# Optimization experiments

Measured on AMD Instinct MI355X. Metric: run time of the kernel, lower is better.

Reference implementation:

```python
import jax, jax.numpy as jnp
import numpy as np

B, CH1, CH2, HID, T, E = 64, 3, 4, 16, 16384, 512

def setup_inputs() -> dict:
    key = jax.random.key(0)
    ks = jax.random.split(key, 12)
    s_t = 1.0 / np.sqrt(T)   # fan_in = input_dim for q/k/v projections
    s_e = 1.0 / np.sqrt(E)   # fan_in = embed_dim for out_proj
    return {
        "x":  jax.random.normal(ks[0], (B, 7, T), jnp.float32),
        "W1": jax.random.normal(ks[1], (HID, CH1), jnp.float32) / np.sqrt(CH1),
        "W2": jax.random.normal(ks[2], (HID, CH2), jnp.float32) / np.sqrt(CH2),
        "Wq": jax.random.normal(ks[3], (E, T), jnp.float32) * s_t,
        "bq": jnp.zeros((E,), jnp.float32),
        "Wk": jax.random.normal(ks[4], (E, T), jnp.float32) * s_t,
        "bk": jnp.zeros((E,), jnp.float32),
        "Wv": jax.random.normal(ks[5], (E, T), jnp.float32) * s_t,
        "bv": jnp.zeros((E,), jnp.float32),
        "Wo": jax.random.normal(ks[6], (T, E), jnp.float32) * s_e,
        "bo": jnp.zeros((T,), jnp.float32),
        "W3": jax.random.normal(ks[7], (CH1, HID), jnp.float32) / np.sqrt(HID),
    }

def reference(x, W1, W2, Wq, bq, Wk, bk, Wv, bv, Wo, bo, W3):
    p = x[:, :CH1]            # [B,3,T]  narrow(1,0,ch_1)
    c = x[:, 3:3 + CH2]       # [B,4,T]  narrow(1,3,ch_2)
    q = jnp.einsum('oc,bct->bot', W1, p)   # fc_1: [B,16,T]
    cc = jnp.einsum('oc,bct->bot', W2, c)  # fc_2: [B,16,T]
    # CrossAttention: Linears act on last dim (T -> E)
    Q = jnp.einsum('bct,et->bce', q, Wq) + bq    # [B,16,E]
    K = jnp.einsum('bct,et->bce', cc, Wk) + bk   # [B,16,E]
    V = jnp.einsum('bct,et->bce', cc, Wv) + bv   # [B,16,E]
    scale = 1.0 / np.sqrt(HID)                   # nch = 16 query channels
    attn_w = jax.nn.softmax(jnp.einsum('bce,bcf->bef', Q, K) * scale, axis=-1)  # [B,E,E]
    attn = jnp.einsum('bef,bcf->bce', attn_w, V)  # [B,16,E]
    out = jnp.einsum('bce,te->bct', attn, Wo) + bo  # out_proj: [B,16,T]
    y = jnp.einsum('oc,bct->bot', W3, out)          # fc_3: [B,3,T]
    return p + y
```

## Files before the change

### kernel.cpp

```cpp
#include <hip/hip_runtime.h>

#define BB 64
#define TT 16384
#define EE 512

#define PSZ 360448
#define PQ_OFF 98304

typedef _Float16 half8 __attribute__((ext_vector_type(8)));
typedef float floatx4 __attribute__((ext_vector_type(4)));

static __device__ __forceinline__ half8 cvt_half8(float4 a, float4 b) {
  half8 h;
  h[0] = (_Float16)a.x; h[1] = (_Float16)a.y; h[2] = (_Float16)a.z; h[3] = (_Float16)a.w;
  h[4] = (_Float16)b.x; h[5] = (_Float16)b.y; h[6] = (_Float16)b.z; h[7] = (_Float16)b.w;
  return h;
}

__global__ __launch_bounds__(512) void proj_gemm(
    const float* __restrict__ x, const float* __restrict__ Wq,
    const float* __restrict__ Wk, const float* __restrict__ Wv,
    float* __restrict__ P, int KL, int NT, int cpx)
{
  __shared__ _Float16 Ah[2][192 * 32];
  __shared__ _Float16 Bh[2][256 * 32];
  const int t = threadIdx.x;
  const int wave = t >> 6, lane = t & 63;
  const int quad = lane >> 4, l16 = lane & 15;
  const int wr = wave >> 2, wc = wave & 3;

  const int orig = blockIdx.x;
  const int logical = (orig & 7) * cpx + (orig >> 3);
  const int chunk = logical / 10;
  const int tile  = logical - chunk * 10;
  const int k0 = chunk * KL;

  const bool isQ = (tile < 2);
  int ntile, mtile, MR, WM, BM, pbase, ldout;
  const float* Wsrc;
  if (isQ) {
    ntile = tile; mtile = 0;
    Wsrc = Wq + (size_t)(ntile * 256) * TT;
    MR = 6; WM = 96; BM = 192; pbase = 0; ldout = 512;
  } else {
    const int t2 = tile - 2;
    mtile = t2 >> 2; ntile = t2 & 3;
    Wsrc = (ntile < 2) ? (Wk + (size_t)(ntile * 256) * TT)
                       : (Wv + (size_t)((ntile - 2) * 256) * TT);
    MR = 4; WM = 64; BM = 128; pbase = PQ_OFF; ldout = 1024;
  }

  const bool aAct = (t < 2 * BM);
  const int arow_s = t >> 1, ah = t & 1;
  const float* aSrc = x;
  if (aAct) {
    const int rg_ = (isQ ? 0 : mtile * 128) + arow_s;
    int b_, j_;
    if (isQ) { b_ = (rg_ * 21846) >> 16; j_ = rg_ - b_ * 3; }
    else     { b_ = rg_ >> 2; j_ = (rg_ & 3) + 3; }
    aSrc = x + (size_t)(b_ * 7 + j_) * TT + k0 + ah * 16;
  }
  const int brow_s = t >> 1, bh = t & 1;
  const float* bSrc = Wsrc + (size_t)brow_s * TT + k0 + bh * 16;

  const int aswr = (arow_s ^ (arow_s >> 2)) & 3;
  const int bswr = (brow_s ^ (brow_s >> 2)) & 3;
  const int aoff0 = arow_s * 32 + ((((ah << 1) | 0) ^ aswr) << 3);
  const int aoff1 = arow_s * 32 + ((((ah << 1) | 1) ^ aswr) << 3);
  const int boff0 = brow_s * 32 + ((((bh << 1) | 0) ^ bswr) << 3);
  const int boff1 = brow_s * 32 + ((((bh << 1) | 1) ^ bswr) << 3);

  floatx4 acc[6][4];
#pragma unroll
  for (int mr = 0; mr < 6; ++mr)
#pragma unroll
    for (int ct = 0; ct < 4; ++ct)
      acc[mr][ct] = (floatx4){0.f, 0.f, 0.f, 0.f};

  float4 la0, la1, la2, la3, lb0, lb1, lb2, lb3;

  auto stage_load = [&](int kt_) {
    const float* ap = aSrc + kt_ * 32;
    const float* bp = bSrc + kt_ * 32;
    if (aAct) {
      la0 = *(const float4*)(ap);
      la1 = *(const float4*)(ap + 4);
      la2 = *(const float4*)(ap + 8);
      la3 = *(const float4*)(ap + 12);
    }
    lb0 = *(const float4*)(bp);
    lb1 = *(const float4*)(bp + 4);
    lb2 = *(const float4*)(bp + 8);
    lb3 = *(const float4*)(bp + 12);
  };
  auto stage_write = [&](int buf_) {
    if (aAct) {
      *(half8*)&Ah[buf_][aoff0] = cvt_half8(la0, la1);
      *(half8*)&Ah[buf_][aoff1] = cvt_half8(la2, la3);
    }
    *(half8*)&Bh[buf_][boff0] = cvt_half8(lb0, lb1);
    *(half8*)&Bh[buf_][boff1] = cvt_half8(lb2, lb3);
  };
  auto compute = [&](int buf_) {
    half8 hb[4];
#pragma unroll
    for (int ct = 0; ct < 4; ++ct) {
      const int br = wc * 64 + ct * 16 + l16;
      const int sb = (br ^ (br >> 2)) & 3;
      hb[ct] = *(const half8*)&Bh[buf_][br * 32 + ((quad ^ sb) << 3)];
    }
#pragma unroll
    for (int mr = 0; mr < 6; ++mr) {
      if (mr < MR) {
        const int ar = wr * WM + mr * 16 + l16;
        const int sa = (ar ^ (ar >> 2)) & 3;
        const half8 ha = *(const half8*)&Ah[buf_][ar * 32 + ((quad ^ sa) << 3)];
#pragma unroll
        for (int ct = 0; ct < 4; ++ct)
          acc[mr][ct] = __builtin_amdgcn_mfma_f32_16x16x32_f16(ha, hb[ct], acc[mr][ct], 0, 0, 0);
      }
    }
  };

  stage_load(0);
  stage_write(0);
  __syncthreads();
  int cur = 0;
  for (int kt = 0; kt < NT; ++kt) {
    if (kt + 1 < NT) stage_load(kt + 1);
    compute(cur);
    if (kt + 1 < NT) {
      stage_write(cur ^ 1);
      __syncthreads();
      cur ^= 1;
    }
  }

  float* outP = P + (size_t)chunk * PSZ + pbase;
#pragma unroll
  for (int mr = 0; mr < 6; ++mr) {
    if (mr < MR) {
#pragma unroll
      for (int ct = 0; ct < 4; ++ct) {
        const int gr = (isQ ? 0 : mtile * 128) + wr * WM + mr * 16 + quad * 4;
        const int gc = ntile * 256 + wc * 64 + ct * 16 + l16;
#pragma unroll
        for (int rg = 0; rg < 4; ++rg)
          outP[(size_t)(gr + rg) * ldout + gc] = acc[mr][ct][rg];
      }
    }
  }
}

__global__ __launch_bounds__(256) void reduce_p(
    const floatx4* __restrict__ P4, float* __restrict__ Xq,
    float* __restrict__ Xkv, int CH)
{
  const int i = blockIdx.x * 256 + threadIdx.x;
  floatx4 s = P4[i];
  for (int c = 1; c < CH; ++c) s += P4[(size_t)c * (PSZ / 4) + i];
  if (i < PQ_OFF / 4) ((floatx4*)Xq)[i] = s;
  else                ((floatx4*)Xkv)[i - PQ_OFF / 4] = s;
}

__global__ __launch_bounds__(256) void attn_mid(
    const float* __restrict__ Xq, const float* __restrict__ Xkv,
    const float* __restrict__ W1, const float* __restrict__ W2,
    const float* __restrict__ W3,
    const float* __restrict__ bq, const float* __restrict__ bk,
    const float* __restrict__ bv, _Float16* __restrict__ U)
{
  __shared__ float Ks[16][512];
  __shared__ float VW[3][512];
  __shared__ float Qs[16][64];
  __shared__ float Xs[4][512];
  __shared__ float W1s[48], W2s[64], W3s[48], W32s[12], w3sum[3];
  const int t = threadIdx.x;
  const int b = blockIdx.y;
  const int e0 = blockIdx.x * 64;

  if (t < 48) W1s[t] = W1[t];
  if (t >= 64 && t < 128) W2s[t - 64] = W2[t - 64];
  if (t >= 128 && t < 176) W3s[t - 128] = W3[t - 128];
  __syncthreads();
  if (t < 12) {
    const int o = t >> 2, jj = t & 3;
    float s = 0.f;
    for (int c = 0; c < 16; ++c) s += W3s[o * 16 + c] * W2s[c * 4 + jj];
    W32s[t] = s;
  }
  if (t >= 16 && t < 19) {
    const int o = t - 16;
    float s = 0.f;
    for (int c = 0; c < 16; ++c) s += W3s[o * 16 + c];
    w3sum[o] = s;
  }
  for (int i = t; i < 2048; i += 256) {
    const int jj = i >> 9, f = i & 511;
    Xs[jj][f] = Xkv[(size_t)(b * 4 + jj) * 1024 + f];
  }
  __syncthreads();
  for (int i = t; i < 8192; i += 256) {
    const int c = i >> 9, f = i & 511;
    float s = bk[f];
#pragma unroll
    for (int jj = 0; jj < 4; ++jj) s += W2s[c * 4 + jj] * Xs[jj][f];
    Ks[c][f] = s;
  }
  __syncthreads();
  for (int i = t; i < 2048; i += 256) {
    const int jj = i >> 9, f = i & 511;
    Xs[jj][f] = Xkv[(size_t)(b * 4 + jj) * 1024 + 512 + f];
  }
  __syncthreads();
  for (int i = t; i < 1536; i += 256) {
    const int o = i >> 9, f = i & 511;
    float s = w3sum[o] * bv[f];
#pragma unroll
    for (int jj = 0; jj < 4; ++jj) s += W32s[o * 4 + jj] * Xs[jj][f];
    VW[o][f] = s;
  }
  for (int i = t; i < 1024; i += 256) {
    const int c = i >> 6, el = i & 63;
    float s = bq[e0 + el];
#pragma unroll
    for (int jj = 0; jj < 3; ++jj)
      s += W1s[c * 3 + jj] * Xq[(size_t)(b * 3 + jj) * 512 + e0 + el];
    Qs[c][el] = s;
  }
  __syncthreads();

  const int wave = t >> 6, lane = t & 63;
  float vwr[3][8];
#pragma unroll
  for (int o = 0; o < 3; ++o) {
    float4 va = *(const float4*)&VW[o][lane * 8];
    float4 vb = *(const float4*)&VW[o][lane * 8 + 4];
    vwr[o][0] = va.x; vwr[o][1] = va.y; vwr[o][2] = va.z; vwr[o][3] = va.w;
    vwr[o][4] = vb.x; vwr[o][5] = vb.y; vwr[o][6] = vb.z; vwr[o][7] = vb.w;
  }

  for (int g = 0; g < 4; ++g) {
    const int el0 = wave * 16 + g * 4;
    float s[4][8];
#pragma unroll
    for (int e = 0; e < 4; ++e)
#pragma unroll
      for (int i = 0; i < 8; ++i) s[e][i] = 0.f;
#pragma unroll
    for (int c = 0; c < 16; ++c) {
      float4 k0 = *(const float4*)&Ks[c][lane * 8];
      float4 k1 = *(const float4*)&Ks[c][lane * 8 + 4];
      float4 qv = *(const float4*)&Qs[c][el0];
      float qa[4] = {qv.x, qv.y, qv.z, qv.w};
#pragma unroll
      for (int e = 0; e < 4; ++e) {
        const float q = qa[e];
        s[e][0] += q * k0.x; s[e][1] += q * k0.y; s[e][2] += q * k0.z; s[e][3] += q * k0.w;
        s[e][4] += q * k1.x; s[e][5] += q * k1.y; s[e][6] += q * k1.z; s[e][7] += q * k1.w;
      }
    }
#pragma unroll
    for (int e = 0; e < 4; ++e) {
      float mx = s[e][0];
#pragma unroll
      for (int i = 1; i < 8; ++i) mx = fmaxf(mx, s[e][i]);
#pragma unroll
      for (int off = 32; off; off >>= 1) mx = fmaxf(mx, __shfl_xor(mx, off));
      float p[8], sum = 0.f;
#pragma unroll
      for (int i = 0; i < 8; ++i) { p[i] = __expf(0.25f * (s[e][i] - mx)); sum += p[i]; }
      float u0 = 0.f, u1 = 0.f, u2 = 0.f;
#pragma unroll
      for (int i = 0; i < 8; ++i) {
        u0 += p[i] * vwr[0][i];
        u1 += p[i] * vwr[1][i];
        u2 += p[i] * vwr[2][i];
      }
#pragma unroll
      for (int off = 32; off; off >>= 1) {
        sum += __shfl_xor(sum, off);
        u0  += __shfl_xor(u0, off);
        u1  += __shfl_xor(u1, off);
        u2  += __shfl_xor(u2, off);
      }
      if (lane == 0) {
        const float inv = 1.0f / sum;
        const size_t base = (size_t)b * 3 * 512 + (e0 + el0 + e);
        U[base]        = (_Float16)(u0 * inv);
        U[base + 512]  = (_Float16)(u1 * inv);
        U[base + 1024] = (_Float16)(u2 * inv);
      }
    }
  }
}

__global__ __launch_bounds__(256) void out_gemm(
    const _Float16* __restrict__ U, const float* __restrict__ Wo,
    const float* __restrict__ x, const float* __restrict__ bo,
    const float* __restrict__ W3, float* __restrict__ outY)
{
  __shared__ _Float16 Au[2][192 * 32];
  __shared__ _Float16 Bw[2][64 * 32];
  const int t = threadIdx.x;
  const int wave = t >> 6, lane = t & 63;
  const int quad = lane >> 4, l16 = lane & 15;
  const int wr = wave >> 1, wc = wave & 1;
  const int ntile = blockIdx.x;

  float w3s[3];
#pragma unroll
  for (int o = 0; o < 3; ++o) {
    float s = 0.f;
#pragma unroll
    for (int c = 0; c < 16; ++c) s += W3[o * 16 + c];
    w3s[o] = s;
  }

  const _Float16* auSrc[3];
  int auoff[3];
#pragma unroll
  for (int r = 0; r < 3; ++r) {
    const int un = t + r * 256;
    const int row = un >> 2, u = un & 3;
    const int sw = (row ^ (row >> 2)) & 3;
    auSrc[r] = U + (size_t)row * EE + u * 8;
    auoff[r] = row * 32 + ((u ^ sw) << 3);
  }
  const bool bAct = (t < 128);
  const int brow_s = t >> 1, bh = t & 1;
  const float* bSrc = Wo + (size_t)(ntile * 64 + brow_s) * EE + bh * 16;
  const int bswr = (brow_s ^ (brow_s >> 2)) & 3;
  const int boff0 = brow_s * 32 + ((((bh << 1) | 0) ^ bswr) << 3);
  const int boff1 = brow_s * 32 + ((((bh << 1) | 1) ^ bswr) << 3);

  floatx4 acc[6][2];
#pragma unroll
  for (int mr = 0; mr < 6; ++mr)
#pragma unroll
    for (int ct = 0; ct < 2; ++ct)
      acc[mr][ct] = (floatx4){0.f, 0.f, 0.f, 0.f};

  half8 lau0, lau1, lau2;
  float4 lb0, lb1, lb2, lb3;

  auto stage_load = [&](int kt_) {
    lau0 = *(const half8*)(auSrc[0] + kt_ * 32);
    lau1 = *(const half8*)(auSrc[1] + kt_ * 32);
    lau2 = *(const half8*)(auSrc[2] + kt_ * 32);
    if (bAct) {
      const float* bp = bSrc + kt_ * 32;
      lb0 = *(const float4*)(bp);
      lb1 = *(const float4*)(bp + 4);
      lb2 = *(const float4*)(bp + 8);
      lb3 = *(const float4*)(bp + 12);
    }
  };
  auto stage_write = [&](int buf_) {
    *(half8*)&Au[buf_][auoff[0]] = lau0;
    *(half8*)&Au[buf_][auoff[1]] = lau1;
    *(half8*)&Au[buf_][auoff[2]] = lau2;
    if (bAct) {
      *(half8*)&Bw[buf_][boff0] = cvt_half8(lb0, lb1);
      *(half8*)&Bw[buf_][boff1] = cvt_half8(lb2, lb3);
    }
  };
  auto compute = [&](int buf_) {
    half8 hb[2];
#pragma unroll
    for (int ct = 0; ct < 2; ++ct) {
      const int br = wc * 32 + ct * 16 + l16;
      const int sb = (br ^ (br >> 2)) & 3;
      hb[ct] = *(const half8*)&Bw[buf_][br * 32 + ((quad ^ sb) << 3)];
    }
#pragma unroll
    for (int mr = 0; mr < 6; ++mr) {
      const int ar = wr * 96 + mr * 16 + l16;
      const int sa = (ar ^ (ar >> 2)) & 3;
      const half8 ha = *(const half8*)&Au[buf_][ar * 32 + ((quad ^ sa) << 3)];
#pragma unroll
      for (int ct = 0; ct < 2; ++ct)
        acc[mr][ct] = __builtin_amdgcn_mfma_f32_16x16x32_f16(ha, hb[ct], acc[mr][ct], 0, 0, 0);
    }
  };

  stage_load(0);
  stage_write(0);
  __syncthreads();
  int cur = 0;
  for (int kt = 0; kt < 16; ++kt) {
    if (kt + 1 < 16) stage_load(kt + 1);
    compute(cur);
    if (kt + 1 < 16) {
      stage_write(cur ^ 1);
      __syncthreads();
      cur ^= 1;
    }
  }

#pragma unroll
  for (int mr = 0; mr < 6; ++mr) {
#pragma unroll
    for (int ct = 0; ct < 2; ++ct) {
      const int tc = ntile * 64 + wc * 32 + ct * 16 + l16;
      const float bot = bo[tc];
#pragma unroll
      for (int rg = 0; rg < 4; ++rg) {
        const int rr = wr * 96 + mr * 16 + quad * 4 + rg;
        const int bb = rr / 3, oo = rr - bb * 3;
        const float v = acc[mr][ct][rg]
                      + x[(size_t)(bb * 7 + oo) * TT + tc]
                      + w3s[oo] * bot;
        outY[(size_t)rr * TT + tc] = v;
      }
    }
  }
}

extern "C" void kernel_launch(void* const* d_in, const int* in_sizes, int n_in,
                              void* d_out, int out_size, void* d_ws, size_t ws_size,
                              hipStream_t stream) {
  const float* x  = (const float*)d_in[0];
  const float* W1 = (const float*)d_in[1];
  const float* W2 = (const float*)d_in[2];
  const float* Wq = (const float*)d_in[3];
  const float* bq = (const float*)d_in[4];
  const float* Wk = (const float*)d_in[5];
  const float* bk = (const float*)d_in[6];
  const float* Wv = (const float*)d_in[7];
  const float* bv = (const float*)d_in[8];
  const float* Wo = (const float*)d_in[9];
  const float* bo = (const float*)d_in[10];
  const float* W3 = (const float*)d_in[11];
  float* out = (float*)d_out;

  char* ws = (char*)d_ws;
  float* Xq      = (float*)ws;
  float* Xkv     = (float*)(ws + 393216);
  _Float16* U    = (_Float16*)(ws + 1441792);
  float* P       = (float*)(ws + 1638400);

  int CH = 32;
  while (CH > 4 && ws_size < 1638400ull + (size_t)CH * PSZ * 4) CH >>= 1;
  const int KL = 16384 / CH;
  const int NT = KL / 32;
  const int nblk = 10 * CH;
  const int cpx = nblk / 8;

  proj_gemm<<<dim3(nblk), 512, 0, stream>>>(x, Wq, Wk, Wv, P, KL, NT, cpx);
  reduce_p<<<dim3(352), 256, 0, stream>>>((const floatx4*)P, Xq, Xkv, CH);
  attn_mid<<<dim3(8, BB), 256, 0, stream>>>(Xq, Xkv, W1, W2, W3, bq, bk, bv, U);
  out_gemm<<<dim3(256), 256, 0, stream>>>(U, Wo, x, bo, W3, out);
}
```

Before: 283.4 us.

## Stream projection GEMM tiles via direct global-to-LDS loads with fp16 partials

The projection GEMM now copies fp32 tiles straight from global memory into XOR-swizzled LDS with global_load_lds, double-buffered with explicit vmcnt waits and barriers. Conversion to fp16 moves to the LDS read side. Blocks grow to 1024 threads and cover all 256 K/V rows, so there are 6 tiles per chunk instead of 10, and A loads are no longer duplicated across m-tiles. Split-K partials are stored as fp16, which halves partial traffic and the reduce work but costs precision in the summed projections and doubles the LDS footprint.

```diff
diff --git a/kernel.cpp b/kernel.cpp
--- a/kernel.cpp
+++ b/kernel.cpp
@@ -17,13 +17,19 @@
   return h;
 }
 
-__global__ __launch_bounds__(512) void proj_gemm(
+static __device__ __forceinline__ void gload_lds16(const void* g, void* l) {
+  __builtin_amdgcn_global_load_lds(
+      (const __attribute__((address_space(1))) void*)g,
+      (__attribute__((address_space(3))) void*)l, 16, 0, 0);
+}
+
+__global__ __launch_bounds__(1024) void proj_gemm(
     const float* __restrict__ x, const float* __restrict__ Wq,
     const float* __restrict__ Wk, const float* __restrict__ Wv,
-    float* __restrict__ P, int KL, int NT, int cpx)
+    _Float16* __restrict__ P, int KL, int NT, int cpx)
 {
-  __shared__ _Float16 Ah[2][192 * 32];
-  __shared__ _Float16 Bh[2][256 * 32];
+  __shared__ float Abuf[2][256 * 32];
+  __shared__ float Bbuf[2][256 * 32];
   const int t = threadIdx.x;
   const int wave = t >> 6, lane = t & 63;
   const int quad = lane >> 4, l16 = lane & 15;
@@ -31,136 +37,139 @@
 
   const int orig = blockIdx.x;
   const int logical = (orig & 7) * cpx + (orig >> 3);
-  const int chunk = logical / 10;
-  const int tile  = logical - chunk * 10;
+  const int chunk = logical / 6;
+  const int tile  = logical - chunk * 6;
   const int k0 = chunk * KL;
 
   const bool isQ = (tile < 2);
-  int ntile, mtile, MR, WM, BM, pbase, ldout;
+  int ntile, MR, WM, BM, pbase, ldout;
   const float* Wsrc;
   if (isQ) {
-    ntile = tile; mtile = 0;
+    ntile = tile;
     Wsrc = Wq + (size_t)(ntile * 256) * TT;
-    MR = 6; WM = 96; BM = 192; pbase = 0; ldout = 512;
+    MR = 3; WM = 48; BM = 192; pbase = 0; ldout = 512;
   } else {
-    const int t2 = tile - 2;
-    mtile = t2 >> 2; ntile = t2 & 3;
+    ntile = tile - 2;
     Wsrc = (ntile < 2) ? (Wk + (size_t)(ntile * 256) * TT)
                        : (Wv + (size_t)((ntile - 2) * 256) * TT);
-    MR = 4; WM = 64; BM = 128; pbase = PQ_OFF; ldout = 1024;
-  }
-
-  const bool aAct = (t < 2 * BM);
-  const int arow_s = t >> 1, ah = t & 1;
-  const float* aSrc = x;
-  if (aAct) {
-    const int rg_ = (isQ ? 0 : mtile * 128) + arow_s;
+    MR = 4; WM = 64; BM = 256; pbase = PQ_OFF; ldout = 1024;
+  }
+
+  const float* aSrc[2];
+  const float* bSrc[2];
+#pragma unroll
+  for (int r = 0; r < 2; ++r) {
+    const int i = r * 1024 + t;
+    const int row0 = i >> 3, u = i & 7;
+    const int row = (row0 < BM) ? row0 : 0;
     int b_, j_;
-    if (isQ) { b_ = (rg_ * 21846) >> 16; j_ = rg_ - b_ * 3; }
-    else     { b_ = rg_ >> 2; j_ = (rg_ & 3) + 3; }
-    aSrc = x + (size_t)(b_ * 7 + j_) * TT + k0 + ah * 16;
-  }
-  const int brow_s = t >> 1, bh = t & 1;
-  const float* bSrc = Wsrc + (size_t)brow_s * TT + k0 + bh * 16;
-
-  const int aswr = (arow_s ^ (arow_s >> 2)) & 3;
-  const int bswr = (brow_s ^ (brow_s >> 2)) & 3;
-  const int aoff0 = arow_s * 32 + ((((ah << 1) | 0) ^ aswr) << 3);
-  const int aoff1 = arow_s * 32 + ((((ah << 1) | 1) ^ aswr) << 3);
-  const int boff0 = brow_s * 32 + ((((bh << 1) | 0) ^ bswr) << 3);
-  const int boff1 = brow_s * 32 + ((((bh << 1) | 1) ^ bswr) << 3);
-
-  floatx4 acc[6][4];
-#pragma unroll
-  for (int mr = 0; mr < 6; ++mr)
+    if (isQ) { b_ = (row * 21846) >> 16; j_ = row - b_ * 3; }
+    else     { b_ = row >> 2; j_ = (row & 3) + 3; }
+    aSrc[r] = x + (size_t)(b_ * 7 + j_) * TT + k0 + ((u ^ (row & 7)) << 2);
+    const int brow = i >> 3, bu = i & 7;
+    bSrc[r] = Wsrc + (size_t)brow * TT + k0 + ((bu ^ (brow & 7)) << 2);
+  }
+
+  floatx4 acc[4][4];
+#pragma unroll
+  for (int mr = 0; mr < 4; ++mr)
 #pragma unroll
     for (int ct = 0; ct < 4; ++ct)
       acc[mr][ct] = (floatx4){0.f, 0.f, 0.f, 0.f};
 
-  float4 la0, la1, la2, la3, lb0, lb1, lb2, lb3;
-
-  auto stage_load = [&](int kt_) {
-    const float* ap = aSrc + kt_ * 32;
-    const float* bp = bSrc + kt_ * 32;
-    if (aAct) {
-      la0 = *(const float4*)(ap);
-      la1 = *(const float4*)(ap + 4);
-      la2 = *(const float4*)(ap + 8);
-      la3 = *(const float4*)(ap + 12);
-    }
-    lb0 = *(const float4*)(bp);
-    lb1 = *(const float4*)(bp + 4);
-    lb2 = *(const float4*)(bp + 8);
-    lb3 = *(const float4*)(bp + 12);
-  };
-  auto stage_write = [&](int buf_) {
-    if (aAct) {
-      *(half8*)&Ah[buf_][aoff0] = cvt_half8(la0, la1);
-      *(half8*)&Ah[buf_][aoff1] = cvt_half8(la2, la3);
-    }
-    *(half8*)&Bh[buf_][boff0] = cvt_half8(lb0, lb1);
-    *(half8*)&Bh[buf_][boff1] = cvt_half8(lb2, lb3);
+  auto stage = [&](int kt_, int buf_) {
+    const int ko = kt_ * 32;
+#pragma unroll
+    for (int r = 0; r < 2; ++r) {
+      gload_lds16(aSrc[r] + ko, &Abuf[buf_][r * 4096 + wave * 256]);
+      gload_lds16(bSrc[r] + ko, &Bbuf[buf_][r * 4096 + wave * 256]);
+    }
   };
   auto compute = [&](int buf_) {
     half8 hb[4];
 #pragma unroll
     for (int ct = 0; ct < 4; ++ct) {
       const int br = wc * 64 + ct * 16 + l16;
-      const int sb = (br ^ (br >> 2)) & 3;
-      hb[ct] = *(const half8*)&Bh[buf_][br * 32 + ((quad ^ sb) << 3)];
-    }
-#pragma unroll
-    for (int mr = 0; mr < 6; ++mr) {
+      const int sb = br & 7;
+      float4 b0 = *(const float4*)&Bbuf[buf_][br * 32 + ((((quad << 1) | 0) ^ sb) << 2)];
+      float4 b1 = *(const float4*)&Bbuf[buf_][br * 32 + ((((quad << 1) | 1) ^ sb) << 2)];
+      hb[ct] = cvt_half8(b0, b1);
+    }
+#pragma unroll
+    for (int mr = 0; mr < 4; ++mr) {
       if (mr < MR) {
         const int ar = wr * WM + mr * 16 + l16;
-        const int sa = (ar ^ (ar >> 2)) & 3;
-        const half8 ha = *(const half8*)&Ah[buf_][ar * 32 + ((quad ^ sa) << 3)];
+        const int sa = ar & 7;
+        float4 a0 = *(const float4*)&Abuf[buf_][ar * 32 + ((((quad << 1) | 0) ^ sa) << 2)];
+        float4 a1 = *(const float4*)&Abuf[buf_][ar * 32 + ((((quad << 1) | 1) ^ sa) << 2)];
+        const half8 ha = cvt_half8(a0, a1);
+        __builtin_amdgcn_s_setprio(1);
 #pragma unroll
         for (int ct = 0; ct < 4; ++ct)
           acc[mr][ct] = __builtin_amdgcn_mfma_f32_16x16x32_f16(ha, hb[ct], acc[mr][ct], 0, 0, 0);
+        __builtin_amdgcn_s_setprio(0);
       }
     }
   };
 
-  stage_load(0);
-  stage_write(0);
-  __syncthreads();
+  stage(0, 0);
+  stage(1, 1);
+  asm volatile("s_waitcnt vmcnt(4)" ::: "memory");
+  __builtin_amdgcn_s_barrier();
+  __builtin_amdgcn_sched_barrier(0);
+
   int cur = 0;
   for (int kt = 0; kt < NT; ++kt) {
-    if (kt + 1 < NT) stage_load(kt + 1);
     compute(cur);
-    if (kt + 1 < NT) {
-      stage_write(cur ^ 1);
-      __syncthreads();
-      cur ^= 1;
-    }
-  }
-
-  float* outP = P + (size_t)chunk * PSZ + pbase;
-#pragma unroll
-  for (int mr = 0; mr < 6; ++mr) {
+    __builtin_amdgcn_s_barrier();
+    if (kt + 2 < NT) {
+      stage(kt + 2, cur);
+      asm volatile("s_waitcnt vmcnt(4)" ::: "memory");
+    } else {
+      asm volatile("s_waitcnt vmcnt(0)" ::: "memory");
+    }
+    __builtin_amdgcn_s_barrier();
+    __builtin_amdgcn_sched_barrier(0);
+    cur ^= 1;
+  }
+
+  _Float16* outP = P + (size_t)chunk * PSZ + pbase;
+#pragma unroll
+  for (int mr = 0; mr < 4; ++mr) {
     if (mr < MR) {
 #pragma unroll
       for (int ct = 0; ct < 4; ++ct) {
-        const int gr = (isQ ? 0 : mtile * 128) + wr * WM + mr * 16 + quad * 4;
+        const int gr = wr * WM + mr * 16 + quad * 4;
         const int gc = ntile * 256 + wc * 64 + ct * 16 + l16;
 #pragma unroll
         for (int rg = 0; rg < 4; ++rg)
-          outP[(size_t)(gr + rg) * ldout + gc] = acc[mr][ct][rg];
+          outP[(size_t)(gr + rg) * ldout + gc] = (_Float16)acc[mr][ct][rg];
       }
     }
   }
 }
 
 __global__ __launch_bounds__(256) void reduce_p(
-    const floatx4* __restrict__ P4, float* __restrict__ Xq,
+    const _Float16* __restrict__ P, float* __restrict__ Xq,
     float* __restrict__ Xkv, int CH)
 {
   const int i = blockIdx.x * 256 + threadIdx.x;
-  floatx4 s = P4[i];
-  for (int c = 1; c < CH; ++c) s += P4[(size_t)c * (PSZ / 4) + i];
-  if (i < PQ_OFF / 4) ((floatx4*)Xq)[i] = s;
-  else                ((floatx4*)Xkv)[i - PQ_OFF / 4] = s;
+  float s[8] = {0.f, 0.f, 0.f, 0.f, 0.f, 0.f, 0.f, 0.f};
+  for (int c = 0; c < CH; ++c) {
+    const half8 v = *(const half8*)(P + (size_t)c * PSZ + (size_t)i * 8);
+#pragma unroll
+    for (int k = 0; k < 8; ++k) s[k] += (float)v[k];
+  }
+  const float4 lo = {s[0], s[1], s[2], s[3]};
+  const float4 hi = {s[4], s[5], s[6], s[7]};
+  if (i < PQ_OFF / 8) {
+    ((float4*)Xq)[i * 2]     = lo;
+    ((float4*)Xq)[i * 2 + 1] = hi;
+  } else {
+    const int j = i - PQ_OFF / 8;
+    ((float4*)Xkv)[j * 2]     = lo;
+    ((float4*)Xkv)[j * 2 + 1] = hi;
+  }
 }
 
 __global__ __launch_bounds__(256) void attn_mid(
@@ -438,17 +447,17 @@
   float* Xq      = (float*)ws;
   float* Xkv     = (float*)(ws + 393216);
   _Float16* U    = (_Float16*)(ws + 1441792);
-  float* P       = (float*)(ws + 1638400);
+  _Float16* P    = (_Float16*)(ws + 1638400);
 
   int CH = 32;
-  while (CH > 4 && ws_size < 1638400ull + (size_t)CH * PSZ * 4) CH >>= 1;
+  while (CH > 4 && ws_size < 1638400ull + (size_t)CH * PSZ * 2) CH >>= 1;
   const int KL = 16384 / CH;
   const int NT = KL / 32;
-  const int nblk = 10 * CH;
+  const int nblk = 6 * CH;
   const int cpx = nblk / 8;
 
-  proj_gemm<<<dim3(nblk), 512, 0, stream>>>(x, Wq, Wk, Wv, P, KL, NT, cpx);
-  reduce_p<<<dim3(352), 256, 0, stream>>>((const floatx4*)P, Xq, Xkv, CH);
+  proj_gemm<<<dim3(nblk), 1024, 0, stream>>>(x, Wq, Wk, Wv, P, KL, NT, cpx);
+  reduce_p<<<dim3(176), 256, 0, stream>>>(P, Xq, Xkv, CH);
   attn_mid<<<dim3(8, BB), 256, 0, stream>>>(Xq, Xkv, W1, W2, W3, bq, bk, bv, U);
   out_gemm<<<dim3(256), 256, 0, stream>>>(U, Wo, x, bo, W3, out);
 }
```

Measured after the change: 259.8 us. 1.09x faster.
